# Optimization experiments

Hardware: AMD Instinct MI355X
Metric: run time of the kernel (lower is better)

The kernel has to match this reference:

```python
import jax, jax.numpy as jnp
import numpy as np

N = 100_000   # nodes
E = 600_000   # edges per layer (avg degree ~6, ogbn-arxiv-like)
IN, H, C = 128, 256, 40


def _sage_layer(x, src, dst, w_self, w_neigh, b):
    """DGL SAGEConv with mean aggregator: fc_self(x) + fc_neigh(mean_nbr) + b."""
    n = x.shape[0]
    msg = x[src]                                               # [E, d] gather
    agg = jax.ops.segment_sum(msg, dst, num_segments=n)        # [N, d]
    deg = jax.ops.segment_sum(jnp.ones((src.shape[0],), x.dtype), dst,
                              num_segments=n)                  # [N]
    h_neigh = agg / jnp.maximum(deg, 1.0)[:, None]             # mean; 0 if isolated
    return x @ w_self.T + h_neigh @ w_neigh.T + b


def setup_inputs() -> dict:
    key = jax.random.key(0)
    ks = jax.random.split(key, 11)
    s = 0.02
    return {
        "x": jax.random.normal(ks[0], (N, IN), jnp.float32),
        "src1": jax.random.randint(ks[1], (E,), 0, N, jnp.int32),
        "dst1": jax.random.randint(ks[2], (E,), 0, N, jnp.int32),
        "src2": jax.random.randint(ks[3], (E,), 0, N, jnp.int32),
        "dst2": jax.random.randint(ks[4], (E,), 0, N, jnp.int32),
        "w_self1": s * jax.random.normal(ks[5], (H, IN), jnp.float32),
        "w_neigh1": s * jax.random.normal(ks[6], (H, IN), jnp.float32),
        "b1": jnp.zeros((H,), jnp.float32),
        "w_self2": s * jax.random.normal(ks[7], (C, H), jnp.float32),
        "w_neigh2": s * jax.random.normal(ks[8], (C, H), jnp.float32),
        "b2": jnp.zeros((C,), jnp.float32),
    }


def reference(x, src1, dst1, src2, dst2, w_self1, w_neigh1, b1,
              w_self2, w_neigh2, b2):
    h = jax.nn.relu(_sage_layer(x, src1, dst1, w_self1, w_neigh1, b1))
    return _sage_layer(h, src2, dst2, w_self2, w_neigh2, b2)
```

## Files before the change

kernel.cpp:

```cpp
#include <hip/hip_runtime.h>
#include <hip/hip_bf16.h>
#include <cstdint>
#include <cstddef>


#define D_IN 128
#define D_H  256
#define D_C  40

#define NBLK     128
#define NBKT_MAX 392
#define BKT_CAP  2560

typedef __bf16 bf16_t;
typedef __attribute__((ext_vector_type(8))) __bf16 bf16x8;
typedef __attribute__((ext_vector_type(4))) __bf16 bf16x4;
typedef __attribute__((ext_vector_type(4))) float  f32x4;

static constexpr size_t NMAX = 100000;
static constexpr size_t EMAX = 600000;
static constexpr size_t NSC_MAX = (size_t)NBKT_MAX * NBLK;
static constexpr size_t alignup(size_t v) { return (v + 255) & ~size_t(255); }

static constexpr size_t HG1_OFF  = 0;
static constexpr size_t HG2_OFF  = alignup(HG1_OFF + NSC_MAX * 4);
static constexpr size_t BS1_OFF  = alignup(HG2_OFF + NSC_MAX * 4);
static constexpr size_t BS2_OFF  = alignup(BS1_OFF + 512 * 4);
static constexpr size_t RP1_OFF  = alignup(BS2_OFF + 512 * 4);
static constexpr size_t RP2_OFF  = alignup(RP1_OFF + (NMAX + 1) * 4);
static constexpr size_t BKT1_OFF = alignup(RP2_OFF + (NMAX + 1) * 4);
static constexpr size_t BKT2_OFF = alignup(BKT1_OFF + EMAX * 4);
static constexpr size_t XCAT_OFF = alignup(BKT2_OFF + EMAX * 4);
static constexpr size_t P_OFF    = alignup(XCAT_OFF + (NMAX + 128) * 256 * 2);
static constexpr size_t W1F_OFF  = alignup(P_OFF + NMAX * 40 * 2);
static constexpr size_t W2F_OFF  = alignup(W1F_OFF + 32 * 256 * 8 * 2);
static constexpr size_t WS_NEEDED = W2F_OFF + 32 * 80 * 8 * 2;

__global__ __launch_bounds__(256) void k_prep(
    const float* __restrict__ x, bf16_t* __restrict__ xcat,
    const float* __restrict__ ws1, const float* __restrict__ wn1,
    const float* __restrict__ ws2, const float* __restrict__ wn2,
    bf16_t* __restrict__ w1f, bf16_t* __restrict__ w2f,
    const int* __restrict__ dst1, const int* __restrict__ dst2,
    int* __restrict__ hg1, int* __restrict__ hg2,
    int N, int E, int chunk, int nbkt, int nconvx) {
  __shared__ int h[NBKT_MAX];
  int bid = blockIdx.x;

  if (bid < nconvx) {
    int t = bid * 256 + threadIdx.x;
    if (t < N * 16) {
      int row = t >> 4, j = t & 15;
      const float* sp = x + (size_t)row * 128 + j * 8;
      float4 v0 = ((const float4*)sp)[0];
      float4 v1 = ((const float4*)sp)[1];
      bf16x8 o;
      o[0] = (bf16_t)v0.x; o[1] = (bf16_t)v0.y; o[2] = (bf16_t)v0.z; o[3] = (bf16_t)v0.w;
      o[4] = (bf16_t)v1.x; o[5] = (bf16_t)v1.y; o[6] = (bf16_t)v1.z; o[7] = (bf16_t)v1.w;
      *(bf16x8*)(xcat + (size_t)row * 256 + j * 8) = o;
    }
    return;
  }
  bid -= nconvx;

  if (bid < 32) {
    int t = bid * 256 + threadIdx.x;
    {
      int ks4g = t >> 8, col = t & 255;
      int k0 = (ks4g >> 2) * 32 + (ks4g & 3) * 8;
      bf16x8 o;
#pragma unroll
      for (int i = 0; i < 8; ++i) {
        int k = k0 + i;
        float v = (k < 128) ? ws1[col * 128 + k] : wn1[col * 128 + (k - 128)];
        o[i] = (bf16_t)v;
      }
      *(bf16x8*)(w1f + (size_t)t * 8) = o;
    }
    if (t < 32 * 80) {
      int ks4g = t / 80, col = t - ks4g * 80;
      int k0 = (ks4g >> 2) * 32 + (ks4g & 3) * 8;
      bf16x8 o;
#pragma unroll
      for (int i = 0; i < 8; ++i) {
        int k = k0 + i;
        float v = (col < 40) ? ws2[col * 256 + k] : wn2[(col - 40) * 256 + k];
        o[i] = (bf16_t)v;
      }
      *(bf16x8*)(w2f + (size_t)t * 8) = o;
    }
    return;
  }
  bid -= 32;
  {
    const int* dst = (bid >> 7) ? dst2 : dst1;
    int*       hg  = (bid >> 7) ? hg2 : hg1;
    int        cb  = bid & 127;
    for (int i = threadIdx.x; i < nbkt; i += 256) h[i] = 0;
    __syncthreads();
    int beg = cb * chunk, end = min(E, beg + chunk);
    for (int e = beg + threadIdx.x; e < end; e += 256)
      atomicAdd(&h[dst[e] >> 8], 1);
    __syncthreads();
    for (int b = threadIdx.x; b < nbkt; b += 256)
      hg[b * NBLK + cb] = h[b];
  }
}

__global__ void k_scan_block(int* __restrict__ a1, int* __restrict__ a2,
                             int* __restrict__ b1s, int* __restrict__ b2s, int n) {
  int* a    = blockIdx.y ? a2 : a1;
  int* bsum = blockIdx.y ? b2s : b1s;
  __shared__ int lds[256];
  int t = threadIdx.x, i = blockIdx.x * 256 + t;
  int v = (i < n) ? a[i] : 0;
  lds[t] = v;
  __syncthreads();
  for (int off = 1; off < 256; off <<= 1) {
    int add = (t >= off) ? lds[t - off] : 0;
    __syncthreads();
    lds[t] += add;
    __syncthreads();
  }
  if (i < n) a[i] = lds[t] - v;
  if (t == 255) bsum[blockIdx.x] = lds[255];
}

__global__ void k_scan_addsums(int* __restrict__ a1, int* __restrict__ a2,
                               const int* __restrict__ b1s, const int* __restrict__ b2s,
                               int n, int nb) {
  int* a          = blockIdx.y ? a2 : a1;
  const int* bsum = blockIdx.y ? b2s : b1s;
  __shared__ int lds[256];
  int t = threadIdx.x;
  int v = (t < nb) ? bsum[t] : 0;
  lds[t] = v;
  __syncthreads();
  for (int off = 1; off < 256; off <<= 1) {
    int add = (t >= off) ? lds[t - off] : 0;
    __syncthreads();
    lds[t] += add;
    __syncthreads();
  }
  __shared__ int excl[256];
  excl[t] = lds[t] - v;
  __syncthreads();
  int i = blockIdx.x * 256 + t;
  if (i < n) a[i] += excl[i >> 8];
}

__global__ void k_scat(const int* __restrict__ src1, const int* __restrict__ dst1,
                       const int* __restrict__ src2, const int* __restrict__ dst2,
                       const int* __restrict__ off1, const int* __restrict__ off2,
                       unsigned* __restrict__ bkt1, unsigned* __restrict__ bkt2,
                       int E, int chunk, int nbkt) {
  const int* src = blockIdx.y ? src2 : src1;
  const int* dst = blockIdx.y ? dst2 : dst1;
  const int* off = blockIdx.y ? off2 : off1;
  unsigned*  bkt = blockIdx.y ? bkt2 : bkt1;
  __shared__ int cur[NBKT_MAX];
  for (int i = threadIdx.x; i < nbkt; i += 256)
    cur[i] = off[i * NBLK + blockIdx.x];
  __syncthreads();
  int beg = blockIdx.x * chunk, end = min(E, beg + chunk);
  for (int e = beg + threadIdx.x; e < end; e += 256) {
    int d = dst[e];
    int slot = atomicAdd(&cur[d >> 8], 1);
    bkt[slot] = (unsigned)src[e] | ((unsigned)(d & 255) << 24);
  }
}

__global__ __launch_bounds__(256) void k_bcsr(
    const int* __restrict__ off1, const int* __restrict__ off2,
    const unsigned* bkt1, const unsigned* bkt2,
    int* csr1, int* csr2,
    int* __restrict__ rp1, int* __restrict__ rp2, int E, int N, int nbkt) {
  const int* off      = blockIdx.y ? off2 : off1;
  const unsigned* bkt = blockIdx.y ? bkt2 : bkt1;
  int* csr            = blockIdx.y ? csr2 : csr1;
  int* rowptr         = blockIdx.y ? rp2 : rp1;

  const int b = blockIdx.x, t = threadIdx.x;
  const int base = off[b * NBLK];
  const int endp = (b == nbkt - 1) ? E : off[(b + 1) * NBLK];
  const int cnt  = endp - base;

  __shared__ int hist[256];
  __shared__ int sc[256];
  __shared__ int cur[256];
  __shared__ int stage[BKT_CAP];

  hist[t] = 0;
  __syncthreads();
  for (int i = t; i < cnt; i += 256)
    atomicAdd(&hist[bkt[base + i] >> 24], 1);
  __syncthreads();

  int v = hist[t];
  sc[t] = v;
  __syncthreads();
  for (int off_ = 1; off_ < 256; off_ <<= 1) {
    int add = (t >= off_) ? sc[t - off_] : 0;
    __syncthreads();
    sc[t] += add;
    __syncthreads();
  }
  int excl = sc[t] - v;

  int node = b * 256 + t;
  if (node < N) rowptr[node] = base + excl;
  if (b == nbkt - 1 && t == 0) rowptr[N] = E;
  cur[t] = excl;
  __syncthreads();

  for (int i = t; i < cnt; i += 256) {
    unsigned u = bkt[base + i];
    int slot = atomicAdd(&cur[u >> 24], 1);
    if (slot < BKT_CAP) stage[slot] = (int)(u & 0xFFFFFFu);
  }
  __syncthreads();
  for (int i = t; i < cnt; i += 256)
    csr[base + i] = stage[i];
}

__global__ void k_agg1(bf16_t* __restrict__ xcat, const int* __restrict__ rowptr,
                       const int* __restrict__ csr, int N) {
  int t = blockIdx.x * 256 + threadIdx.x;
  int node = t >> 4, l = t & 15;
  if (node >= N) return;
  int beg = rowptr[node], end = rowptr[node + 1];
  float acc[8] = {0.f, 0.f, 0.f, 0.f, 0.f, 0.f, 0.f, 0.f};
  int e = beg;
  for (; e + 4 <= end; e += 4) {
    int s0 = csr[e], s1 = csr[e + 1], s2 = csr[e + 2], s3 = csr[e + 3];
    bf16x8 v0 = *(const bf16x8*)(xcat + (size_t)s0 * 256 + l * 8);
    bf16x8 v1 = *(const bf16x8*)(xcat + (size_t)s1 * 256 + l * 8);
    bf16x8 v2 = *(const bf16x8*)(xcat + (size_t)s2 * 256 + l * 8);
    bf16x8 v3 = *(const bf16x8*)(xcat + (size_t)s3 * 256 + l * 8);
#pragma unroll
    for (int i = 0; i < 8; ++i)
      acc[i] += (float)v0[i] + (float)v1[i] + (float)v2[i] + (float)v3[i];
  }
  for (; e < end; ++e) {
    int s = csr[e];
    bf16x8 v = *(const bf16x8*)(xcat + (size_t)s * 256 + l * 8);
#pragma unroll
    for (int i = 0; i < 8; ++i) acc[i] += (float)v[i];
  }
  float rd = (end > beg) ? 1.0f / (float)(end - beg) : 0.0f;
  bf16x8 o;
#pragma unroll
  for (int i = 0; i < 8; ++i) o[i] = (bf16_t)(acc[i] * rd);
  *(bf16x8*)(xcat + (size_t)node * 256 + 128 + l * 8) = o;
}

__global__ __launch_bounds__(256, 3) void k_fused(
    const bf16_t* __restrict__ xcat, const bf16_t* __restrict__ w1f,
    const float* __restrict__ b1, const bf16_t* __restrict__ w2f,
    const float* __restrict__ b2v, float* __restrict__ out,
    bf16_t* __restrict__ p, int N) {
  __shared__ __align__(16) char lds[32768];
  const int tid  = (int)threadIdx.x;
  const int wv   = tid >> 6;
  const int lane = tid & 63;
  const int lr   = lane & 15;
  const int lg   = lane >> 4;
  const int c0   = wv * 64;
  const int m0   = (int)blockIdx.x * 64;

  {
    const char* tb = (const char*)(xcat + (size_t)m0 * 256);
#pragma unroll
    for (int i = 0; i < 8; ++i) {
      int L   = i * 4096 + tid * 16;
      int row = L >> 9;
      int c   = L & 511;
      int so  = (row << 9) | (c ^ ((row & 7) << 4));
      __builtin_amdgcn_global_load_lds(
          (const __attribute__((address_space(1))) void*)(tb + so),
          (__attribute__((address_space(3))) void*)(lds + L), 16, 0, 0);
    }
  }

  bf16x8 wfc[4];
#pragma unroll
  for (int wb = 0; wb < 4; ++wb)
    wfc[wb] = *(const bf16x8*)(w1f + ((size_t)(0 * 4 + lg) * 256 +
                                      (c0 + wb * 16 + lr)) * 8);
  __syncthreads();

  bf16x8 axc[4];
#pragma unroll
  for (int rb = 0; rb < 4; ++rb) {
    int lrow = rb * 16 + lr;
    axc[rb] = *(const bf16x8*)(lds + lrow * 512 +
                               ((0 * 64 + lg * 16) ^ ((lrow & 7) << 4)));
  }

  f32x4 acc[4][4] = {};
#pragma unroll
  for (int ks = 0; ks < 8; ++ks) {
    bf16x8 wfn[4], axn[4];
    if (ks < 7) {
#pragma unroll
      for (int wb = 0; wb < 4; ++wb)
        wfn[wb] = *(const bf16x8*)(w1f + ((size_t)((ks + 1) * 4 + lg) * 256 +
                                          (c0 + wb * 16 + lr)) * 8);
#pragma unroll
      for (int rb = 0; rb < 4; ++rb) {
        int lrow = rb * 16 + lr;
        axn[rb] = *(const bf16x8*)(lds + lrow * 512 +
                                   (((ks + 1) * 64 + lg * 16) ^ ((lrow & 7) << 4)));
      }
    }
#pragma unroll
    for (int wb = 0; wb < 4; ++wb)
#pragma unroll
      for (int rb = 0; rb < 4; ++rb)
        acc[wb][rb] = __builtin_amdgcn_mfma_f32_16x16x32_bf16(
            wfc[wb], axc[rb], acc[wb][rb], 0, 0, 0);
    if (ks < 7) {
#pragma unroll
      for (int i = 0; i < 4; ++i) { wfc[i] = wfn[i]; axc[i] = axn[i]; }
    }
  }

  __syncthreads();

#pragma unroll
  for (int wb = 0; wb < 4; ++wb) {
    float4 b4 = *(const float4*)(b1 + c0 + wb * 16 + lg * 4);
#pragma unroll
    for (int rb = 0; rb < 4; ++rb) {
      int xrow = rb * 16 + lr;
      bf16x4 o;
      o[0] = (bf16_t)fmaxf(acc[wb][rb][0] + b4.x, 0.f);
      o[1] = (bf16_t)fmaxf(acc[wb][rb][1] + b4.y, 0.f);
      o[2] = (bf16_t)fmaxf(acc[wb][rb][2] + b4.z, 0.f);
      o[3] = (bf16_t)fmaxf(acc[wb][rb][3] + b4.w, 0.f);
      *(bf16x4*)(lds + xrow * 512 +
                 ((c0 * 2 + wb * 32 + lg * 8) ^ ((xrow & 7) << 4))) = o;
    }
  }
  __syncthreads();

  const int arow = wv * 16 + lr;
  bf16x8 hfc = *(const bf16x8*)(lds + arow * 512 +
                                ((0 * 64 + lg * 16) ^ ((arow & 7) << 4)));
  bf16x8 w2c[5];
#pragma unroll
  for (int wb = 0; wb < 5; ++wb)
    w2c[wb] = *(const bf16x8*)(w2f + ((size_t)(0 * 4 + lg) * 80 +
                                      (wb * 16 + lr)) * 8);

  f32x4 acc2[5] = {};
#pragma unroll
  for (int ks = 0; ks < 8; ++ks) {
    bf16x8 hfn, w2n[5];
    if (ks < 7) {
      hfn = *(const bf16x8*)(lds + arow * 512 +
                             (((ks + 1) * 64 + lg * 16) ^ ((arow & 7) << 4)));
#pragma unroll
      for (int wb = 0; wb < 5; ++wb)
        w2n[wb] = *(const bf16x8*)(w2f + ((size_t)((ks + 1) * 4 + lg) * 80 +
                                          (wb * 16 + lr)) * 8);
    }
#pragma unroll
    for (int wb = 0; wb < 5; ++wb)
      acc2[wb] = __builtin_amdgcn_mfma_f32_16x16x32_bf16(
          w2c[wb], hfc, acc2[wb], 0, 0, 0);
    if (ks < 7) {
      hfc = hfn;
#pragma unroll
      for (int i = 0; i < 5; ++i) w2c[i] = w2n[i];
    }
  }

  const int r = m0 + wv * 16 + lr;
  if (r < N) {
#pragma unroll
    for (int wb = 0; wb < 5; ++wb) {
      int col0 = wb * 16 + lg * 4;
      f32x4 v = acc2[wb];
      if (col0 < 40) {
        float4 b4 = *(const float4*)(b2v + col0);
        v[0] += b4.x; v[1] += b4.y; v[2] += b4.z; v[3] += b4.w;
        *(f32x4*)(out + (size_t)r * 40 + col0) = v;
      } else {
        bf16x4 o;
        o[0] = (bf16_t)v[0]; o[1] = (bf16_t)v[1];
        o[2] = (bf16_t)v[2]; o[3] = (bf16_t)v[3];
        *(bf16x4*)(p + (size_t)r * 40 + (col0 - 40)) = o;
      }
    }
  }
}

__global__ void k_agg2fin(const bf16_t* __restrict__ p, const int* __restrict__ rowptr,
                          const int* __restrict__ csr, float* __restrict__ out, int N) {
  int t = blockIdx.x * 256 + threadIdx.x;
  int node = t / 10, l = t - node * 10;
  if (node >= N) return;
  int beg = rowptr[node], end = rowptr[node + 1];
  float a0 = 0.f, a1 = 0.f, a2 = 0.f, a3 = 0.f;
  int e = beg;
  for (; e + 4 <= end; e += 4) {
    int s0 = csr[e], s1 = csr[e + 1], s2 = csr[e + 2], s3 = csr[e + 3];
    bf16x4 v0 = *(const bf16x4*)(p + (size_t)s0 * 40 + l * 4);
    bf16x4 v1 = *(const bf16x4*)(p + (size_t)s1 * 40 + l * 4);
    bf16x4 v2 = *(const bf16x4*)(p + (size_t)s2 * 40 + l * 4);
    bf16x4 v3 = *(const bf16x4*)(p + (size_t)s3 * 40 + l * 4);
    a0 += (float)v0[0] + (float)v1[0] + (float)v2[0] + (float)v3[0];
    a1 += (float)v0[1] + (float)v1[1] + (float)v2[1] + (float)v3[1];
    a2 += (float)v0[2] + (float)v1[2] + (float)v2[2] + (float)v3[2];
    a3 += (float)v0[3] + (float)v1[3] + (float)v2[3] + (float)v3[3];
  }
  for (; e < end; ++e) {
    int s = csr[e];
    bf16x4 v = *(const bf16x4*)(p + (size_t)s * 40 + l * 4);
    a0 += (float)v[0]; a1 += (float)v[1]; a2 += (float)v[2]; a3 += (float)v[3];
  }
  float rd = (end > beg) ? 1.0f / (float)(end - beg) : 0.0f;
  float* o = out + (size_t)node * 40 + l * 4;
  float4 cur = *(const float4*)o;
  cur.x += a0 * rd;
  cur.y += a1 * rd;
  cur.z += a2 * rd;
  cur.w += a3 * rd;
  *(float4*)o = cur;
}

extern "C" void kernel_launch(void* const* d_in, const int* in_sizes, int n_in,
                              void* d_out, int out_size, void* d_ws, size_t ws_size,
                              hipStream_t stream) {
  const float* x    = (const float*)d_in[0];
  const int*   src1 = (const int*)d_in[1];
  const int*   dst1 = (const int*)d_in[2];
  const int*   src2 = (const int*)d_in[3];
  const int*   dst2 = (const int*)d_in[4];
  const float* ws1  = (const float*)d_in[5];
  const float* wn1  = (const float*)d_in[6];
  const float* b1   = (const float*)d_in[7];
  const float* ws2  = (const float*)d_in[8];
  const float* wn2  = (const float*)d_in[9];
  const float* b2   = (const float*)d_in[10];
  float*       out  = (float*)d_out;

  const int N = in_sizes[0] / D_IN;
  const int E = in_sizes[1];
  if (ws_size < WS_NEEDED) return;

  char*     ws   = (char*)d_ws;
  int*      hg1  = (int*)(ws + HG1_OFF);
  int*      hg2  = (int*)(ws + HG2_OFF);
  int*      bs1  = (int*)(ws + BS1_OFF);
  int*      bs2  = (int*)(ws + BS2_OFF);
  int*      rp1  = (int*)(ws + RP1_OFF);
  int*      rp2  = (int*)(ws + RP2_OFF);
  unsigned* bkt1 = (unsigned*)(ws + BKT1_OFF);
  unsigned* bkt2 = (unsigned*)(ws + BKT2_OFF);
  int*      csr1 = (int*)(ws + BKT1_OFF);
  int*      csr2 = (int*)(ws + BKT2_OFF);
  bf16_t*   xcat = (bf16_t*)(ws + XCAT_OFF);
  bf16_t*   p    = (bf16_t*)(ws + P_OFF);
  bf16_t*   w1f  = (bf16_t*)(ws + W1F_OFF);
  bf16_t*   w2f  = (bf16_t*)(ws + W2F_OFF);

  const int nbkt  = (N + 255) >> 8;
  const int chunk = (E + NBLK - 1) / NBLK;
  const int nsc   = nbkt * NBLK;
  const int nscb  = (nsc + 255) / 256;
  const int nconvx = (N * 16 + 255) / 256;
  const int ntiles = (N + 63) / 64;

  k_prep<<<nconvx + 32 + 2 * NBLK, 256, 0, stream>>>(
      x, xcat, ws1, wn1, ws2, wn2, w1f, w2f, dst1, dst2, hg1, hg2,
      N, E, chunk, nbkt, nconvx);

  k_scan_block<<<dim3(nscb, 2), 256, 0, stream>>>(hg1, hg2, bs1, bs2, nsc);
  k_scan_addsums<<<dim3(nscb, 2), 256, 0, stream>>>(hg1, hg2, bs1, bs2, nsc, nscb);
  k_scat<<<dim3(NBLK, 2), 256, 0, stream>>>(src1, dst1, src2, dst2, hg1, hg2,
                                            bkt1, bkt2, E, chunk, nbkt);
  k_bcsr<<<dim3(nbkt, 2), 256, 0, stream>>>(hg1, hg2, bkt1, bkt2, csr1, csr2,
                                            rp1, rp2, E, N, nbkt);

  k_agg1<<<(N * 16 + 255) / 256, 256, 0, stream>>>(xcat, rp1, csr1, N);
  k_fused<<<ntiles, 256, 0, stream>>>(xcat, w1f, b1, w2f, b2, out, p, N);
  k_agg2fin<<<(N * 10 + 255) / 256, 256, 0, stream>>>(p, rp2, csr2, out, N);
}
```

Baseline: 136.5 us.

## Fold block-sum scan into scatter/CSR kernels and predicate aggregation tails

Removes the separate k_scan_addsums launch by having k_scat and k_bcsr each rescan the per-block sums in LDS and add the exclusive prefix on the fly. This saves one kernel launch and a read-modify-write pass over the histogram, at the cost of redundant small scans in every block. The aggregation kernels also replace the scalar remainder loop with a masked 4-wide loop that clamps indices and zero-weights the padding lanes, keeping memory-level parallelism for the tail. The xcat padding is reduced as well.

```diff
diff --git a/kernel.cpp b/kernel.cpp
--- a/kernel.cpp
+++ b/kernel.cpp
@@ -31,7 +31,7 @@
 static constexpr size_t BKT1_OFF = alignup(RP2_OFF + (NMAX + 1) * 4);
 static constexpr size_t BKT2_OFF = alignup(BKT1_OFF + EMAX * 4);
 static constexpr size_t XCAT_OFF = alignup(BKT2_OFF + EMAX * 4);
-static constexpr size_t P_OFF    = alignup(XCAT_OFF + (NMAX + 128) * 256 * 2);
+static constexpr size_t P_OFF    = alignup(XCAT_OFF + (NMAX + 64) * 256 * 2);
 static constexpr size_t W1F_OFF  = alignup(P_OFF + NMAX * 40 * 2);
 static constexpr size_t W2F_OFF  = alignup(W1F_OFF + 32 * 256 * 8 * 2);
 static constexpr size_t WS_NEEDED = W2F_OFF + 32 * 80 * 8 * 2;
@@ -126,44 +126,42 @@
   if (t == 255) bsum[blockIdx.x] = lds[255];
 }
 
-__global__ void k_scan_addsums(int* __restrict__ a1, int* __restrict__ a2,
-                               const int* __restrict__ b1s, const int* __restrict__ b2s,
-                               int n, int nb) {
-  int* a          = blockIdx.y ? a2 : a1;
-  const int* bsum = blockIdx.y ? b2s : b1s;
-  __shared__ int lds[256];
-  int t = threadIdx.x;
-  int v = (t < nb) ? bsum[t] : 0;
-  lds[t] = v;
-  __syncthreads();
-  for (int off = 1; off < 256; off <<= 1) {
-    int add = (t >= off) ? lds[t - off] : 0;
-    __syncthreads();
-    lds[t] += add;
-    __syncthreads();
-  }
-  __shared__ int excl[256];
-  excl[t] = lds[t] - v;
-  __syncthreads();
-  int i = blockIdx.x * 256 + t;
-  if (i < n) a[i] += excl[i >> 8];
-}
-
 __global__ void k_scat(const int* __restrict__ src1, const int* __restrict__ dst1,
                        const int* __restrict__ src2, const int* __restrict__ dst2,
-                       const int* __restrict__ off1, const int* __restrict__ off2,
+                       const int* __restrict__ hg1, const int* __restrict__ hg2,
+                       const int* __restrict__ b1s, const int* __restrict__ b2s,
                        unsigned* __restrict__ bkt1, unsigned* __restrict__ bkt2,
-                       int E, int chunk, int nbkt) {
+                       int E, int chunk, int nbkt, int nb) {
   const int* src = blockIdx.y ? src2 : src1;
   const int* dst = blockIdx.y ? dst2 : dst1;
-  const int* off = blockIdx.y ? off2 : off1;
+  const int* hg  = blockIdx.y ? hg2 : hg1;
+  const int* bs  = blockIdx.y ? b2s : b1s;
   unsigned*  bkt = blockIdx.y ? bkt2 : bkt1;
+  const int cb = blockIdx.x, t = threadIdx.x;
+
+  __shared__ int sbuf[256];
+  __shared__ int sexcl[256];
   __shared__ int cur[NBKT_MAX];
-  for (int i = threadIdx.x; i < nbkt; i += 256)
-    cur[i] = off[i * NBLK + blockIdx.x];
-  __syncthreads();
-  int beg = blockIdx.x * chunk, end = min(E, beg + chunk);
-  for (int e = beg + threadIdx.x; e < end; e += 256) {
+
+  int v = (t < nb) ? bs[t] : 0;
+  sbuf[t] = v;
+  __syncthreads();
+  for (int off = 1; off < 256; off <<= 1) {
+    int add = (t >= off) ? sbuf[t - off] : 0;
+    __syncthreads();
+    sbuf[t] += add;
+    __syncthreads();
+  }
+  sexcl[t] = sbuf[t] - v;
+  __syncthreads();
+  for (int i = t; i < nbkt; i += 256) {
+    int idx = i * NBLK + cb;
+    cur[i] = hg[idx] + sexcl[idx >> 8];
+  }
+  __syncthreads();
+
+  int beg = cb * chunk, end = min(E, beg + chunk);
+  for (int e = beg + t; e < end; e += 256) {
     int d = dst[e];
     int slot = atomicAdd(&cur[d >> 8], 1);
     bkt[slot] = (unsigned)src[e] | ((unsigned)(d & 255) << 24);
@@ -171,27 +169,52 @@
 }
 
 __global__ __launch_bounds__(256) void k_bcsr(
-    const int* __restrict__ off1, const int* __restrict__ off2,
+    const int* __restrict__ hg1, const int* __restrict__ hg2,
+    const int* __restrict__ b1s, const int* __restrict__ b2s,
     const unsigned* bkt1, const unsigned* bkt2,
     int* csr1, int* csr2,
-    int* __restrict__ rp1, int* __restrict__ rp2, int E, int N, int nbkt) {
-  const int* off      = blockIdx.y ? off2 : off1;
+    int* __restrict__ rp1, int* __restrict__ rp2, int E, int N, int nbkt, int nb) {
+  const int* hg       = blockIdx.y ? hg2 : hg1;
+  const int* bs       = blockIdx.y ? b2s : b1s;
   const unsigned* bkt = blockIdx.y ? bkt2 : bkt1;
   int* csr            = blockIdx.y ? csr2 : csr1;
   int* rowptr         = blockIdx.y ? rp2 : rp1;
 
   const int b = blockIdx.x, t = threadIdx.x;
-  const int base = off[b * NBLK];
-  const int endp = (b == nbkt - 1) ? E : off[(b + 1) * NBLK];
-  const int cnt  = endp - base;
-
+
+  __shared__ int sbuf[256];
   __shared__ int hist[256];
   __shared__ int sc[256];
   __shared__ int cur[256];
   __shared__ int stage[BKT_CAP];
-
+  __shared__ int s_base, s_endp;
+
+  int v0 = (t < nb) ? bs[t] : 0;
+  sbuf[t] = v0;
+  __syncthreads();
+  for (int off_ = 1; off_ < 256; off_ <<= 1) {
+    int add = (t >= off_) ? sbuf[t - off_] : 0;
+    __syncthreads();
+    sbuf[t] += add;
+    __syncthreads();
+  }
+  if (t == 0) {
+    int i0 = b * NBLK;
+    int e0 = sbuf[i0 >> 8] - ((i0 >> 8) < nb ? bs[i0 >> 8] : 0);
+    s_base = hg[i0] + e0;
+    if (b == nbkt - 1) {
+      s_endp = E;
+    } else {
+      int i1 = (b + 1) * NBLK;
+      int e1 = sbuf[i1 >> 8] - ((i1 >> 8) < nb ? bs[i1 >> 8] : 0);
+      s_endp = hg[i1] + e1;
+    }
+  }
   hist[t] = 0;
   __syncthreads();
+  const int base = s_base, endp = s_endp;
+  const int cnt  = endp - base;
+
   for (int i = t; i < cnt; i += 256)
     atomicAdd(&hist[bkt[base + i] >> 24], 1);
   __syncthreads();
@@ -230,22 +253,21 @@
   if (node >= N) return;
   int beg = rowptr[node], end = rowptr[node + 1];
   float acc[8] = {0.f, 0.f, 0.f, 0.f, 0.f, 0.f, 0.f, 0.f};
-  int e = beg;
-  for (; e + 4 <= end; e += 4) {
-    int s0 = csr[e], s1 = csr[e + 1], s2 = csr[e + 2], s3 = csr[e + 3];
+  for (int e = beg; e < end; e += 4) {
+    int e1 = e + 1 < end ? e + 1 : e;
+    int e2 = e + 2 < end ? e + 2 : e;
+    int e3 = e + 3 < end ? e + 3 : e;
+    float m1 = e + 1 < end ? 1.f : 0.f;
+    float m2 = e + 2 < end ? 1.f : 0.f;
+    float m3 = e + 3 < end ? 1.f : 0.f;
+    int s0 = csr[e], s1 = csr[e1], s2 = csr[e2], s3 = csr[e3];
     bf16x8 v0 = *(const bf16x8*)(xcat + (size_t)s0 * 256 + l * 8);
     bf16x8 v1 = *(const bf16x8*)(xcat + (size_t)s1 * 256 + l * 8);
     bf16x8 v2 = *(const bf16x8*)(xcat + (size_t)s2 * 256 + l * 8);
     bf16x8 v3 = *(const bf16x8*)(xcat + (size_t)s3 * 256 + l * 8);
 #pragma unroll
     for (int i = 0; i < 8; ++i)
-      acc[i] += (float)v0[i] + (float)v1[i] + (float)v2[i] + (float)v3[i];
-  }
-  for (; e < end; ++e) {
-    int s = csr[e];
-    bf16x8 v = *(const bf16x8*)(xcat + (size_t)s * 256 + l * 8);
-#pragma unroll
-    for (int i = 0; i < 8; ++i) acc[i] += (float)v[i];
+      acc[i] += (float)v0[i] + m1 * (float)v1[i] + m2 * (float)v2[i] + m3 * (float)v3[i];
   }
   float rd = (end > beg) ? 1.0f / (float)(end - beg) : 0.0f;
   bf16x8 o;
@@ -403,22 +425,22 @@
   if (node >= N) return;
   int beg = rowptr[node], end = rowptr[node + 1];
   float a0 = 0.f, a1 = 0.f, a2 = 0.f, a3 = 0.f;
-  int e = beg;
-  for (; e + 4 <= end; e += 4) {
-    int s0 = csr[e], s1 = csr[e + 1], s2 = csr[e + 2], s3 = csr[e + 3];
+  for (int e = beg; e < end; e += 4) {
+    int e1 = e + 1 < end ? e + 1 : e;
+    int e2 = e + 2 < end ? e + 2 : e;
+    int e3 = e + 3 < end ? e + 3 : e;
+    float m1 = e + 1 < end ? 1.f : 0.f;
+    float m2 = e + 2 < end ? 1.f : 0.f;
+    float m3 = e + 3 < end ? 1.f : 0.f;
+    int s0 = csr[e], s1 = csr[e1], s2 = csr[e2], s3 = csr[e3];
     bf16x4 v0 = *(const bf16x4*)(p + (size_t)s0 * 40 + l * 4);
     bf16x4 v1 = *(const bf16x4*)(p + (size_t)s1 * 40 + l * 4);
     bf16x4 v2 = *(const bf16x4*)(p + (size_t)s2 * 40 + l * 4);
     bf16x4 v3 = *(const bf16x4*)(p + (size_t)s3 * 40 + l * 4);
-    a0 += (float)v0[0] + (float)v1[0] + (float)v2[0] + (float)v3[0];
-    a1 += (float)v0[1] + (float)v1[1] + (float)v2[1] + (float)v3[1];
-    a2 += (float)v0[2] + (float)v1[2] + (float)v2[2] + (float)v3[2];
-    a3 += (float)v0[3] + (float)v1[3] + (float)v2[3] + (float)v3[3];
-  }
-  for (; e < end; ++e) {
-    int s = csr[e];
-    bf16x4 v = *(const bf16x4*)(p + (size_t)s * 40 + l * 4);
-    a0 += (float)v[0]; a1 += (float)v[1]; a2 += (float)v[2]; a3 += (float)v[3];
+    a0 += (float)v0[0] + m1 * (float)v1[0] + m2 * (float)v2[0] + m3 * (float)v3[0];
+    a1 += (float)v0[1] + m1 * (float)v1[1] + m2 * (float)v2[1] + m3 * (float)v3[1];
+    a2 += (float)v0[2] + m1 * (float)v1[2] + m2 * (float)v2[2] + m3 * (float)v3[2];
+    a3 += (float)v0[3] + m1 * (float)v1[3] + m2 * (float)v2[3] + m3 * (float)v3[3];
   }
   float rd = (end > beg) ? 1.0f / (float)(end - beg) : 0.0f;
   float* o = out + (size_t)node * 40 + l * 4;
@@ -478,11 +500,10 @@
       N, E, chunk, nbkt, nconvx);
 
   k_scan_block<<<dim3(nscb, 2), 256, 0, stream>>>(hg1, hg2, bs1, bs2, nsc);
-  k_scan_addsums<<<dim3(nscb, 2), 256, 0, stream>>>(hg1, hg2, bs1, bs2, nsc, nscb);
   k_scat<<<dim3(NBLK, 2), 256, 0, stream>>>(src1, dst1, src2, dst2, hg1, hg2,
-                                            bkt1, bkt2, E, chunk, nbkt);
-  k_bcsr<<<dim3(nbkt, 2), 256, 0, stream>>>(hg1, hg2, bkt1, bkt2, csr1, csr2,
-                                            rp1, rp2, E, N, nbkt);
+                                            bs1, bs2, bkt1, bkt2, E, chunk, nbkt, nscb);
+  k_bcsr<<<dim3(nbkt, 2), 256, 0, stream>>>(hg1, hg2, bs1, bs2, bkt1, bkt2,
+                                            csr1, csr2, rp1, rp2, E, N, nbkt, nscb);
 
   k_agg1<<<(N * 16 + 255) / 256, 256, 0, stream>>>(xcat, rp1, csr1, N);
   k_fused<<<ntiles, 256, 0, stream>>>(xcat, w1f, b1, w2f, b2, out, p, N);
```

After: 133.2 us, median of 2. -2.4%, faster.
